# Optimization experiments

Measured on AMD Instinct MI355X. Metric: run time of the kernel, lower is better.

## Reference

```python
import jax, jax.numpy as jnp
import numpy as np

LSP_ORDER = 32
RATE = 0.01
N_ITER = 4
MIN_D = RATE * np.pi / (LSP_ORDER + 1)  # _precompute


def setup_inputs() -> dict:
    key = jax.random.key(0)
    # LSP coefficients in radians, valid range (0, pi)
    w = jax.random.uniform(key, (256, 4096, LSP_ORDER + 1), dtype=jnp.float32,
                           minval=0.0, maxval=float(np.pi))
    return {"w": w}


def reference(w):
    min_d = jnp.asarray(MIN_D, w.dtype)
    pi = jnp.asarray(np.pi, w.dtype)
    K, w1 = w[..., :1], w[..., 1:]  # (..., 1), (..., M)

    def one_pass(w1):
        # Sequential left-to-right repair: each pair (m, m+1) is pushed apart
        # by half the deficit; the updated right element feeds the next step.
        wt = jnp.moveaxis(w1, -1, 0)  # (M, ...)

        def step(c, nxt):
            s = 0.5 * jnp.maximum(min_d - (nxt - c), 0.0)
            return nxt + s, c - s  # carry = updated w1[m+1], out = final w1[m]

        c_last, outs = jax.lax.scan(step, wt[0], wt[1:])
        w1n = jnp.concatenate([outs, c_last[None]], axis=0)  # (M, ...)
        return jnp.clip(jnp.moveaxis(w1n, 0, -1), min_d, pi - min_d)

    # Early-exit break in the original is a no-op once converged (step sizes
    # become 0 and clip is idempotent), so running all N_ITER is exact.
    for _ in range(N_ITER):
        w1 = one_pass(w1)

    return jnp.concatenate([K, w1], axis=-1)
```

## Files before the change

### kernel.cpp

```cpp
#include <hip/hip_runtime.h>
#include <math.h>


#define ROWS_PER_BLOCK 256
#define ROW 33
#define FPB (ROWS_PER_BLOCK * ROW)
#define V4PB (FPB / 4)

__global__ __launch_bounds__(256) void lsp_stability_kernel(
    const float* __restrict__ in, float* __restrict__ out)
{
    __shared__ float smem[FPB];
    const int tid = threadIdx.x;
    const long long base = (long long)blockIdx.x * FPB;

    const float4* __restrict__ in4 = (const float4*)(in + base);
    float4* __restrict__ out4 = (float4*)(out + base);
    float4* s4 = (float4*)smem;

#pragma unroll
    for (int j = 0; j < 8; ++j)
        s4[tid + j * 256] = in4[tid + j * 256];
    if (tid < (V4PB - 2048))
        s4[2048 + tid] = in4[2048 + tid];
    __syncthreads();

    const float MIND = (float)(0.01 * M_PI / 33.0);
    const float PI_F = (float)M_PI;
    const float HI = PI_F - MIND;

    float w[32];
    float* row = smem + tid * ROW;
#pragma unroll
    for (int k = 0; k < 32; ++k) w[k] = row[k + 1];

#pragma unroll
    for (int it = 0; it < 4; ++it) {
        float c = w[0];
#pragma unroll
        for (int k = 1; k < 32; ++k) {
            float nxt = w[k];
            float sft = 0.5f * fmaxf(MIND - (nxt - c), 0.0f);
            w[k - 1] = c - sft;
            c = nxt + sft;
        }
        w[31] = c;
#pragma unroll
        for (int k = 0; k < 32; ++k)
            w[k] = fminf(fmaxf(w[k], MIND), HI);
    }

#pragma unroll
    for (int k = 0; k < 32; ++k) row[k + 1] = w[k];
    __syncthreads();

#pragma unroll
    for (int j = 0; j < 8; ++j)
        out4[tid + j * 256] = s4[tid + j * 256];
    if (tid < (V4PB - 2048))
        out4[2048 + tid] = s4[2048 + tid];
}

extern "C" void kernel_launch(void* const* d_in, const int* in_sizes, int n_in,
                              void* d_out, int out_size, void* d_ws, size_t ws_size,
                              hipStream_t stream) {
    const float* in = (const float*)d_in[0];
    float* out = (float*)d_out;
    const int blocks = in_sizes[0] / FPB;
    lsp_stability_kernel<<<blocks, ROWS_PER_BLOCK, 0, stream>>>(in, out);
}
```

Before: 239.2 us.

## Double-buffer tiles with async global-to-LDS DMA in single-wave persistent blocks

Each block is now a single 64-lane wavefront that works through 8 tiles of 64 rows. Tiles are loaded with global_load_lds async DMA into a double-buffered LDS array, and the next tile's load overlaps compute on the current one. Manual s_waitcnt vmcnt counts replace __syncthreads. The goal is to hide global load latency and cut barrier overhead, at the cost of fragile hand-tuned waitcnt values and fewer threads per block. Stores still go out synchronously from LDS, and a prefetch write into the buffer that is still being stored may race with it.

```diff
diff --git a/kernel.cpp b/kernel.cpp
--- a/kernel.cpp
+++ b/kernel.cpp
@@ -2,63 +2,83 @@
 #include <math.h>
 
 
-#define ROWS_PER_BLOCK 256
 #define ROW 33
-#define FPB (ROWS_PER_BLOCK * ROW)
-#define V4PB (FPB / 4)
+#define LANES 64
+#define TILE_F (LANES * ROW)
+#define TILE_V4 (TILE_F / 4)
+#define TPB 8
 
-__global__ __launch_bounds__(256) void lsp_stability_kernel(
+typedef const __attribute__((address_space(1))) unsigned int* gas_p;
+typedef __attribute__((address_space(3))) unsigned int* las_p;
+
+__device__ __forceinline__ void dma_tile(gas_p g, las_p s, int lane) {
+#pragma unroll
+    for (int j = 0; j < 8; ++j)
+        __builtin_amdgcn_global_load_lds(g + (size_t)(lane + j * 64) * 4,
+                                         s + (size_t)(lane + j * 64) * 4,
+                                         16, 0, 0);
+    if (lane < (TILE_V4 - 512))
+        __builtin_amdgcn_global_load_lds(g + (size_t)(lane + 512) * 4,
+                                         s + (size_t)(lane + 512) * 4,
+                                         16, 0, 0);
+}
+
+__global__ __launch_bounds__(64) void lsp_stability_kernel(
     const float* __restrict__ in, float* __restrict__ out)
 {
-    __shared__ float smem[FPB];
-    const int tid = threadIdx.x;
-    const long long base = (long long)blockIdx.x * FPB;
+    __shared__ alignas(16) float smem[2][TILE_F];
+    const int lane = threadIdx.x;
+    const long long t0 = (long long)blockIdx.x * TPB;
 
-    const float4* __restrict__ in4 = (const float4*)(in + base);
-    float4* __restrict__ out4 = (float4*)(out + base);
-    float4* s4 = (float4*)smem;
+    const float MIND = (float)(0.01 * M_PI / 33.0);
+    const float HI = (float)M_PI - MIND;
+
+    dma_tile((gas_p)(in + t0 * TILE_F), (las_p)&smem[0][0], lane);
+
+#pragma unroll 1
+    for (int i = 0; i < TPB; ++i) {
+        if (i + 1 < TPB)
+            dma_tile((gas_p)(in + (t0 + i + 1) * TILE_F),
+                     (las_p)&smem[(i + 1) & 1][0], lane);
+
+        if (i == 0)            asm volatile("s_waitcnt vmcnt(9)" ::: "memory");
+        else if (i + 1 < TPB)  asm volatile("s_waitcnt vmcnt(18)" ::: "memory");
+        else                   asm volatile("s_waitcnt vmcnt(9)" ::: "memory");
+
+        float* buf = smem[i & 1];
+        float* row = buf + lane * ROW;
+
+        float w[32];
+#pragma unroll
+        for (int k = 0; k < 32; ++k) w[k] = row[k + 1];
 
 #pragma unroll
-    for (int j = 0; j < 8; ++j)
-        s4[tid + j * 256] = in4[tid + j * 256];
-    if (tid < (V4PB - 2048))
-        s4[2048 + tid] = in4[2048 + tid];
-    __syncthreads();
-
-    const float MIND = (float)(0.01 * M_PI / 33.0);
-    const float PI_F = (float)M_PI;
-    const float HI = PI_F - MIND;
-
-    float w[32];
-    float* row = smem + tid * ROW;
+        for (int it = 0; it < 4; ++it) {
+            float c = w[0];
 #pragma unroll
-    for (int k = 0; k < 32; ++k) w[k] = row[k + 1];
+            for (int k = 1; k < 32; ++k) {
+                float nxt = w[k];
+                float sft = 0.5f * fmaxf(MIND - (nxt - c), 0.0f);
+                w[k - 1] = c - sft;
+                c = nxt + sft;
+            }
+            w[31] = c;
+#pragma unroll
+            for (int k = 0; k < 32; ++k)
+                w[k] = fminf(fmaxf(w[k], MIND), HI);
+        }
 
 #pragma unroll
-    for (int it = 0; it < 4; ++it) {
-        float c = w[0];
+        for (int k = 0; k < 32; ++k) row[k + 1] = w[k];
+
+        float4* o4 = (float4*)(out + (t0 + i) * TILE_F);
+        const float4* b4 = (const float4*)buf;
 #pragma unroll
-        for (int k = 1; k < 32; ++k) {
-            float nxt = w[k];
-            float sft = 0.5f * fmaxf(MIND - (nxt - c), 0.0f);
-            w[k - 1] = c - sft;
-            c = nxt + sft;
-        }
-        w[31] = c;
-#pragma unroll
-        for (int k = 0; k < 32; ++k)
-            w[k] = fminf(fmaxf(w[k], MIND), HI);
+        for (int j = 0; j < 8; ++j)
+            o4[lane + j * 64] = b4[lane + j * 64];
+        if (lane < (TILE_V4 - 512))
+            o4[lane + 512] = b4[lane + 512];
     }
-
-#pragma unroll
-    for (int k = 0; k < 32; ++k) row[k + 1] = w[k];
-    __syncthreads();
-
-#pragma unroll
-    for (int j = 0; j < 8; ++j)
-        out4[tid + j * 256] = s4[tid + j * 256];
-    if (tid < (V4PB - 2048))
-        out4[2048 + tid] = s4[2048 + tid];
 }
 
 extern "C" void kernel_launch(void* const* d_in, const int* in_sizes, int n_in,
@@ -66,6 +86,6 @@
                               hipStream_t stream) {
     const float* in = (const float*)d_in[0];
     float* out = (float*)d_out;
-    const int blocks = in_sizes[0] / FPB;
-    lsp_stability_kernel<<<blocks, ROWS_PER_BLOCK, 0, stream>>>(in, out);
+    const int blocks = in_sizes[0] / (TILE_F * TPB);
+    lsp_stability_kernel<<<blocks, LANES, 0, stream>>>(in, out);
 }
```

After: 244.6 us. 2.3% more time.
